# Kernel optimization log

Measured on AMD Instinct MI355X. Metric: run time of the kernel, lower is better.

The kernel has to match this reference:

```python
import jax, jax.numpy as jnp
import numpy as np

BS, S, D, H, HS, HSEL, L = 32, 512, 512, 8, 2, 4, 6
DK = D // H  # 64
HD = H - HS  # dynamic heads


def setup_inputs() -> dict:
    key = jax.random.key(0)
    ks = jax.random.split(key, 10)
    w = lambda k, shape: jax.random.normal(k, shape, dtype=jnp.float32) * 0.02
    return {
        'q_embed_data': jax.random.normal(ks[0], (BS, S, D), jnp.float32),
        'qa_embed_data': jax.random.normal(ks[1], (BS, S, D), jnp.float32),
        # stacked per-layer params (torch Linear convention: W[out,in], y = x@W.T+b)
        'Wq': w(ks[2], (L, D, D)), 'bq': jnp.zeros((L, D), jnp.float32),
        'Wv': w(ks[3], (L, D, D)), 'bv': jnp.zeros((L, D), jnp.float32),
        'Wg': w(ks[4], (L, HD, D)),                      # routing gate, no bias
        'Wo': w(ks[5], (L, D, D)), 'bo': jnp.zeros((L, D), jnp.float32),
        'ln1_g': jnp.ones((L, D), jnp.float32), 'ln1_b': jnp.zeros((L, D), jnp.float32),
        'W1': w(ks[6], (L, D, D)), 'b1': jnp.zeros((L, D), jnp.float32),
        'W2': w(ks[7], (L, D, D)), 'b2': jnp.zeros((L, D), jnp.float32),
        'ln2_g': jnp.ones((L, D), jnp.float32), 'ln2_b': jnp.zeros((L, D), jnp.float32),
    }


def _layer_norm(x, g, b):
    m = x.mean(-1, keepdims=True)
    v = ((x - m) ** 2).mean(-1, keepdims=True)
    return (x - m) * jax.lax.rsqrt(v + 1e-5) * g + b


def _moh_attention(xq, xv, Wq, bq, Wv, bv, Wg, Wo, bo, strict):
    bs, s, d = xq.shape
    q = xq @ Wq.T + bq            # kq_same=True: k = q projection
    v = xv @ Wv.T + bv
    qh = q.reshape(bs, s, H, DK).transpose(0, 2, 1, 3)   # [b,h,s,dk]
    vh = v.reshape(bs, s, H, DK).transpose(0, 2, 1, 3)
    scores = jnp.einsum('bhqd,bhkd->bhqk', qh, qh) / jnp.sqrt(jnp.float32(DK))
    # mask==1 -> causal incl. diag; mask==0 -> strictly causal
    allow = jnp.tril(jnp.ones((s, s), bool), k=-1 if strict else 0)
    scores = jnp.where(allow, scores, jnp.float32(-1e9))
    # pad-zero shift: first query row replaced by zeros -> uniform attention
    scores = scores.at[:, :, 0, :].set(0.0)
    # per-token top-k head routing over dynamic heads
    gates = jax.nn.softmax(q.reshape(bs * s, D) @ Wg.T, axis=-1)  # [bs*s, HD]
    _, idx = jax.lax.top_k(gates, HSEL)
    dmask = jnp.zeros_like(gates).at[jnp.arange(bs * s)[:, None], idx].set(1.0)
    dyn = (gates * dmask).reshape(bs, s, HD)
    routing = jnp.concatenate([jnp.ones((bs, s, HS), gates.dtype), dyn], -1).mean(1)  # [b,H]
    attn = jax.nn.softmax(scores, axis=-1)
    ctx = jnp.einsum('bhqk,bhkd->bhqd', attn, vh) * routing[:, :, None, None]
    out = ctx.transpose(0, 2, 1, 3).reshape(bs, s, D) @ Wo.T + bo
    f = dmask.sum(0)
    P = gates.mean(0)
    balance = jnp.sum((f / (f.sum() + 1e-5)) * (P / (P.sum() + 1e-5)))
    return out, balance


def reference(q_embed_data, qa_embed_data, Wq, bq, Wv, bv, Wg, Wo, bo,
              ln1_g, ln1_b, W1, b1, W2, b2, ln2_g, ln2_b):
    def layer(i, xq, xv, strict):
        a, bl = _moh_attention(xq, xv, Wq[i], bq[i], Wv[i], bv[i], Wg[i], Wo[i], bo[i], strict)
        x = _layer_norm(xq + a, ln1_g[i], ln1_b[i])
        ffn = jax.nn.relu(x @ W1[i].T + b1[i]) @ W2[i].T + b2[i]
        return _layer_norm(x + ffn, ln2_g[i], ln2_b[i]), bl

    y = qa_embed_data
    x = q_embed_data
    # blocks_1: self-attention on y, mask=1
    y, _ = layer(0, y, y, False)
    y, _ = layer(1, y, y, False)
    # blocks_2: alternate mask=1 self-attn / mask=0 cross-attn (values=y)
    x, _ = layer(2, x, x, False)
    x, bl = layer(3, x, y, True)
    x, _ = layer(4, x, x, False)
    x, bl = layer(5, x, y, True)
    return (x, bl)
```

## Files before the change

### kernel.cpp

```cpp
#include <hip/hip_runtime.h>
#include <cstdint>

#define BSZ 32
#define SEQ 512
#define DM  512
#define NH  8
#define DK  64
#define HS_ 2
#define HD_ 6
#define NL  6
#define MROWS (BSZ*SEQ)
#define QVLD 1024
#define SCL 0.18033688011112043f

typedef unsigned short bf16_t;
typedef __attribute__((ext_vector_type(4))) float f32x4;
typedef __attribute__((ext_vector_type(8))) short bf16x8;
typedef __attribute__((ext_vector_type(8))) unsigned short u16x8;

#define DEV static __device__ __forceinline__

DEV float bf2f(bf16_t b) {
  unsigned int u = ((unsigned int)b) << 16;
  float f; __builtin_memcpy(&f, &u, 4); return f;
}
DEV bf16_t f2b(float f) {
  unsigned int u; __builtin_memcpy(&u, &f, 4);
  unsigned int r = (u + 0x7fffu + ((u >> 16) & 1u)) >> 16;
  return (bf16_t)r;
}
DEV void unp2(unsigned int w, float& a, float& b) {
  unsigned int ua = w << 16, ub = w & 0xffff0000u;
  __builtin_memcpy(&a, &ua, 4); __builtin_memcpy(&b, &ub, 4);
}
DEV unsigned cvtpk(float lo, float hi) {
  unsigned r;
  asm("v_cvt_pk_bf16_f32 %0, %1, %2" : "=v"(r) : "v"(lo), "v"(hi));
  return r;
}

DEV void gload_lds16(const bf16_t* g, bf16_t* l) {
  __builtin_amdgcn_global_load_lds(
      (const __attribute__((address_space(1))) void*)g,
      (__attribute__((address_space(3))) void*)l, 16, 0, 0);
}

DEV bf16x8 scale_q(bf16x8 v) {
  u16x8 u;
  __builtin_memcpy(&u, &v, 16);
  unsigned w[4];
#pragma unroll
  for (int e = 0; e < 4; ++e)
    w[e] = cvtpk(bf2f(u[2 * e]) * SCL, bf2f(u[2 * e + 1]) * SCL);
  bf16x8 r;
  __builtin_memcpy(&r, w, 16);
  return r;
}

__global__ __launch_bounds__(256) void f2b2_kernel(
    const float* __restrict__ s0, const float* __restrict__ s1,
    bf16_t* __restrict__ d0, bf16_t* __restrict__ d1) {
  const float* s = blockIdx.y ? s1 : s0;
  bf16_t* d = blockIdx.y ? d1 : d0;
  const int i = blockIdx.x * 256 + threadIdx.x;
  float4 v = reinterpret_cast<const float4*>(s)[i];
  ushort4 o;
  o.x = f2b(v.x); o.y = f2b(v.y); o.z = f2b(v.z); o.w = f2b(v.w);
  reinterpret_cast<ushort4*>(d)[i] = o;
}

__global__ __launch_bounds__(256) void f2bw_kernel(
    const float* __restrict__ s0, const float* __restrict__ s1,
    const float* __restrict__ s2, const float* __restrict__ s3,
    const float* __restrict__ s4, bf16_t* __restrict__ dst) {
  const float* srcs[5] = {s0, s1, s2, s3, s4};
  const float* s = srcs[blockIdx.y];
  bf16_t* d = dst + (size_t)blockIdx.y * ((size_t)NL * DM * DM);
  const int i = blockIdx.x * 256 + threadIdx.x;
  float4 v = reinterpret_cast<const float4*>(s)[i];
  ushort4 o;
  o.x = f2b(v.x); o.y = f2b(v.y); o.z = f2b(v.z); o.w = f2b(v.w);
  reinterpret_cast<ushort4*>(d)[i] = o;
}

template <int NB, int NWG, bool RELU>
__global__ __launch_bounds__(512) void gemm8(
    const bf16_t* __restrict__ A0, const bf16_t* __restrict__ A1,
    const bf16_t* __restrict__ W0, const bf16_t* __restrict__ W1,
    const float* __restrict__ b0, const float* __restrict__ b1,
    bf16_t* __restrict__ Yb, int ldy) {
  const int K = 512;
  const int lin = blockIdx.y * NB + blockIdx.x;
  const int cpx = NWG / 8;
  const int swz = (lin & 7) * cpx + (lin >> 3);
  const int bn = swz % NB, bm = swz / NB;
  const int tid = threadIdx.x, wid = tid >> 6, lane = tid & 63;
  const int wr = wid >> 2, wc = wid & 3;
  const int lrow = lane & 15, grp = lane >> 4;
  const int l3 = lane >> 3, c3 = lane & 7;

  __shared__ __align__(16) bf16_t Lds[3][24576];

  const bool hi = (bn * 256) >= 512;
  const bf16_t* Asel = hi ? A1 : A0;
  const bf16_t* Wsel = hi ? (W1 - (size_t)512 * K) : W0;
  const float* bsel = hi ? (b1 - 512) : b0;

  f32x4 acc[4][4];
#pragma unroll
  for (int m = 0; m < 4; ++m)
#pragma unroll
    for (int n = 0; n < 4; ++n) acc[m][n] = f32x4{0.f, 0.f, 0.f, 0.f};

  const char* LB = (const char*)Lds;

  auto stage3 = [&](int kt, int buf, int half) {
#pragma unroll
    for (int cc = 0; cc < 3; ++cc) {
      const int c = wid + (half * 3 + cc) * 8;
      const int colb = ((c3 ^ l3) * 8);
      if (c < 16) {
        gload_lds16(Asel + (size_t)(bm * 128 + c * 8 + l3) * K + kt * 64 + colb,
                    &Lds[buf][c * 512]);
      } else {
        const int cb = c - 16;
        gload_lds16(Wsel + (size_t)(bn * 256 + cb * 8 + l3) * K + kt * 64 + colb,
                    &Lds[buf][8192 + cb * 512]);
      }
    }
  };
  auto rdA = [&](int buf, int rA, int ks) -> bf16x8 {
    const int off = buf * 49152 + rA * 128 + ((ks * 64 + grp * 16) ^ ((rA & 7) << 4));
    return *reinterpret_cast<const bf16x8*>(LB + off);
  };
  auto rdB = [&](int buf, int rB, int ks) -> bf16x8 {
    const int off = buf * 49152 + 16384 + rB * 128 + ((ks * 64 + grp * 16) ^ ((rB & 7) << 4));
    return *reinterpret_cast<const bf16x8*>(LB + off);
  };

  stage3(0, 0, 0); stage3(0, 0, 1);
  stage3(1, 1, 0); stage3(1, 1, 1);
  asm volatile("s_waitcnt vmcnt(6)" ::: "memory");
  __builtin_amdgcn_s_barrier();

  for (int g = 0; g < 8; ++g) {
    const int bufR = g % 3, bufW = (g + 2) % 3;
    const bool st = g < 6;
    bf16x8 bwv[4][2], afv[2][2];
#pragma unroll
    for (int n = 0; n < 4; ++n)
#pragma unroll
      for (int ks = 0; ks < 2; ++ks)
        bwv[n][ks] = rdB(bufR, wc * 64 + n * 16 + lrow, ks);
#pragma unroll
    for (int m = 0; m < 2; ++m)
#pragma unroll
      for (int ks = 0; ks < 2; ++ks)
        afv[m][ks] = rdA(bufR, wr * 64 + m * 16 + lrow, ks);
    if (st) stage3(g + 2, bufW, 0);
    __builtin_amdgcn_s_barrier();
    asm volatile("s_waitcnt lgkmcnt(0)" ::: "memory");
    __builtin_amdgcn_s_setprio(1);
#pragma unroll
    for (int ks = 0; ks < 2; ++ks)
#pragma unroll
      for (int m = 0; m < 2; ++m)
#pragma unroll
        for (int n = 0; n < 4; ++n)
          acc[m][n] = __builtin_amdgcn_mfma_f32_16x16x32_bf16(afv[m][ks], bwv[n][ks], acc[m][n], 0, 0, 0);
    __builtin_amdgcn_s_setprio(0);
    __builtin_amdgcn_s_barrier();
#pragma unroll
    for (int m = 0; m < 2; ++m)
#pragma unroll
      for (int ks = 0; ks < 2; ++ks)
        afv[m][ks] = rdA(bufR, wr * 64 + 32 + m * 16 + lrow, ks);
    if (st) stage3(g + 2, bufW, 1);
    __builtin_amdgcn_s_barrier();
    asm volatile("s_waitcnt lgkmcnt(0)" ::: "memory");
    __builtin_amdgcn_s_setprio(1);
#pragma unroll
    for (int ks = 0; ks < 2; ++ks)
#pragma unroll
      for (int m = 0; m < 2; ++m)
#pragma unroll
        for (int n = 0; n < 4; ++n)
          acc[2 + m][n] = __builtin_amdgcn_mfma_f32_16x16x32_bf16(afv[m][ks], bwv[n][ks], acc[2 + m][n], 0, 0, 0);
    __builtin_amdgcn_s_setprio(0);
    if (g < 6) {
      asm volatile("s_waitcnt vmcnt(6)" ::: "memory");
    } else if (g == 6) {
      asm volatile("s_waitcnt vmcnt(0)" ::: "memory");
    }
    __builtin_amdgcn_s_barrier();
  }

  const int r0 = bm * 128 + wr * 64 + grp * 4;
  const int c0 = bn * 256 + wc * 64 + lrow;
#pragma unroll
  for (int n = 0; n < 4; ++n) {
    const int col = c0 + n * 16;
    const float bc = bsel[col];
#pragma unroll
    for (int qm = 0; qm < 4; ++qm)
#pragma unroll
      for (int j = 0; j < 4; ++j) {
        float v = acc[qm][n][j] + bc;
        if (RELU) v = fmaxf(v, 0.f);
        Yb[(size_t)(r0 + qm * 16 + j) * ldy + col] = f2b(v);
      }
  }
}

__global__ __launch_bounds__(256) void gates_kernel(
    const bf16_t* __restrict__ qv, const float* __restrict__ Wg,
    float* __restrict__ rdyn, float* __restrict__ fP) {
  __shared__ float wg_s[HD_ * DM];
  __shared__ float blk[4][18];
  const int tid = threadIdx.x, wid = tid >> 6, lane = tid & 63;
  for (int i = tid; i < HD_ * DM / 4; i += 256)
    reinterpret_cast<float4*>(wg_s)[i] = reinterpret_cast<const float4*>(Wg)[i];
  __syncthreads();
  const int bb = blockIdx.x >> 4;
  const int t0 = (blockIdx.x & 15) * 32 + wid * 8;
  float fs[6] = {0, 0, 0, 0, 0, 0}, ps[6] = {0, 0, 0, 0, 0, 0}, rs[6] = {0, 0, 0, 0, 0, 0};
  for (int it = 0; it < 8; ++it) {
    const int tok = bb * SEQ + t0 + it;
    uint4 u = reinterpret_cast<const uint4*>(qv + (size_t)tok * QVLD)[lane];
    float x[8];
    unp2(u.x, x[0], x[1]); unp2(u.y, x[2], x[3]);
    unp2(u.z, x[4], x[5]); unp2(u.w, x[6], x[7]);
    float g[6];
#pragma unroll
    for (int j = 0; j < 6; ++j) {
      float p = 0.f;
#pragma unroll
      for (int e = 0; e < 8; ++e) p = fmaf(x[e], wg_s[j * DM + lane * 8 + e], p);
#pragma unroll
      for (int off = 32; off; off >>= 1) p += __shfl_xor(p, off);
      g[j] = p;
    }
    float mx = g[0];
#pragma unroll
    for (int j = 1; j < 6; ++j) mx = fmaxf(mx, g[j]);
    float se = 0.f;
#pragma unroll
    for (int j = 0; j < 6; ++j) { g[j] = __expf(g[j] - mx); se += g[j]; }
    float inv = 1.f / se;
#pragma unroll
    for (int j = 0; j < 6; ++j) g[j] *= inv;
    int d1 = 0;
#pragma unroll
    for (int j = 1; j < 6; ++j)
      if (g[j] < g[d1] || (g[j] == g[d1] && j > d1)) d1 = j;
    int d2 = (d1 == 0) ? 1 : 0;
#pragma unroll
    for (int j = 0; j < 6; ++j) {
      if (j == d1) continue;
      if (g[j] < g[d2] || (g[j] == g[d2] && j > d2)) d2 = j;
    }
#pragma unroll
    for (int j = 0; j < 6; ++j) {
      const bool drop = (j == d1) || (j == d2);
      fs[j] += drop ? 0.f : 1.f;
      ps[j] += g[j];
      rs[j] += drop ? 0.f : g[j];
    }
  }
  if (lane == 0) {
#pragma unroll
    for (int j = 0; j < 6; ++j) {
      blk[wid][j] = fs[j]; blk[wid][6 + j] = ps[j]; blk[wid][12 + j] = rs[j];
    }
  }
  __syncthreads();
  if (tid < 18) {
    float s = blk[0][tid] + blk[1][tid] + blk[2][tid] + blk[3][tid];
    if (tid < 12) atomicAdd(&fP[tid], s);
    else atomicAdd(&rdyn[bb * 6 + (tid - 12)], s * (1.f / 512.f));
  }
}

__global__ __launch_bounds__(256, 2) void fattn_kernel(
    const bf16_t* __restrict__ qv, const float* __restrict__ rdyn,
    bf16_t* __restrict__ ctx, int strict) {
  const int bh = blockIdx.x, qt = blockIdx.y;
  const int b = bh >> 3, h = bh & 7;
  const int tid = threadIdx.x, wid = tid >> 6, lane = tid & 63;
  const int c0 = lane & 15, grp = lane >> 4;
  const int l3 = lane >> 3, c3 = lane & 7;
  const int kidx = lane & 31, dhalf = lane >> 5;

  __shared__ __align__(16) bf16_t Ks[64 * 64];
  __shared__ __align__(16) bf16_t Vt[64 * 72];
  __shared__ __align__(16) bf16_t Ps[4][32 * 64];
  __shared__ float csum[64];

  const bf16_t* qp = qv;
  const bf16_t* vp = qv + 512;
  const float factor = (h < HS_) ? 1.f : rdyn[b * 6 + (h - HS_)];

  const int qbase = qt * 128 + wid * 32;

  bf16x8 qf[2][2];
#pragma unroll
  for (int nt = 0; nt < 2; ++nt)
#pragma unroll
    for (int ks = 0; ks < 2; ++ks)
      qf[nt][ks] = scale_q(*reinterpret_cast<const bf16x8*>(
          qp + ((size_t)(b * SEQ + qbase + nt * 16 + c0)) * QVLD + h * DK + ks * 32 + grp * 8));

  f32x4 acc[2][4];
#pragma unroll
  for (int m = 0; m < 2; ++m)
#pragma unroll
    for (int d = 0; d < 4; ++d) acc[m][d] = f32x4{0.f, 0.f, 0.f, 0.f};
  float mreg[2] = {-3e38f, -3e38f};
  float lreg[2] = {0.f, 0.f};
  float cs[8] = {0, 0, 0, 0, 0, 0, 0, 0};

  const int lastk = (qbase + 31 - strict) >> 6;
  const int ktmax = 2 * qt + 1;

  for (int kt = 0; kt <= ktmax; ++kt) {
#pragma unroll
    for (int i = 0; i < 2; ++i) {
      int row = i * 32 + wid * 8 + l3;
      int blk = c3 ^ l3;
      gload_lds16(qp + ((size_t)(b * SEQ + kt * 64 + row)) * QVLD + h * DK + blk * 8,
                  Ks + (i * 32 + wid * 8) * 64);
    }
#pragma unroll
    for (int j = 0; j < 2; ++j) {
      const int d0 = (wid * 2 + j) * 8 + dhalf * 4;
      const bf16_t* src = vp + ((size_t)(b * SEQ + kt * 64 + 2 * kidx)) * QVLD + h * DK + d0;
      ushort4 lo = *reinterpret_cast<const ushort4*>(src);
      ushort4 hv = *reinterpret_cast<const ushort4*>(src + QVLD);
      *reinterpret_cast<unsigned*>(&Vt[(d0 + 0) * 72 + 2 * kidx]) = (unsigned)lo.x | ((unsigned)hv.x << 16);
      *reinterpret_cast<unsigned*>(&Vt[(d0 + 1) * 72 + 2 * kidx]) = (unsigned)lo.y | ((unsigned)hv.y << 16);
      *reinterpret_cast<unsigned*>(&Vt[(d0 + 2) * 72 + 2 * kidx]) = (unsigned)lo.z | ((unsigned)hv.z << 16);
      *reinterpret_cast<unsigned*>(&Vt[(d0 + 3) * 72 + 2 * kidx]) = (unsigned)lo.w | ((unsigned)hv.w << 16);
      if (qt == 3) {
        cs[j * 4 + 0] += bf2f(lo.x) + bf2f(hv.x);
        cs[j * 4 + 1] += bf2f(lo.y) + bf2f(hv.y);
        cs[j * 4 + 2] += bf2f(lo.z) + bf2f(hv.z);
        cs[j * 4 + 3] += bf2f(lo.w) + bf2f(hv.w);
      }
    }
    __syncthreads();

    if (kt <= lastk) {
      const char* KsB = (const char*)Ks;
      bf16x8 kf[4][2];
#pragma unroll
      for (int mt = 0; mt < 4; ++mt)
#pragma unroll
        for (int ks = 0; ks < 2; ++ks)
          kf[mt][ks] = *reinterpret_cast<const bf16x8*>(
              KsB + (mt * 16 + c0) * 128 + 16 * ((4 * ks + grp) ^ (c0 & 7)));
      f32x4 s[4][2];
#pragma unroll
      for (int mt = 0; mt < 4; ++mt)
#pragma unroll
        for (int nt = 0; nt < 2; ++nt) s[mt][nt] = f32x4{0.f, 0.f, 0.f, 0.f};
      __builtin_amdgcn_s_setprio(1);
#pragma unroll
      for (int mt = 0; mt < 4; ++mt)
#pragma unroll
        for (int nt = 0; nt < 2; ++nt)
#pragma unroll
          for (int ks = 0; ks < 2; ++ks)
            s[mt][nt] = __builtin_amdgcn_mfma_f32_16x16x32_bf16(
                kf[mt][ks], qf[nt][ks], s[mt][nt], 0, 0, 0);
      __builtin_amdgcn_s_setprio(0);

      const bool masked = (kt == lastk);
      if (masked) {
#pragma unroll
        for (int nt = 0; nt < 2; ++nt) {
          const int q = qbase + nt * 16 + c0;
#pragma unroll
          for (int mt = 0; mt < 4; ++mt)
#pragma unroll
            for (int j = 0; j < 4; ++j) {
              int k = kt * 64 + mt * 16 + grp * 4 + j;
              if (k + strict > q) s[mt][nt][j] = -1e30f;
            }
        }
      }
      float mx[2];
#pragma unroll
      for (int nt = 0; nt < 2; ++nt) {
        float a = fmaxf(s[0][nt][0], s[0][nt][1]);
        a = fmaxf(fmaxf(a, s[0][nt][2]), s[0][nt][3]);
        float bm_ = fmaxf(s[1][nt][0], s[1][nt][1]);
        bm_ = fmaxf(fmaxf(bm_, s[1][nt][2]), s[1][nt][3]);
        float c = fmaxf(s[2][nt][0], s[2][nt][1]);
        c = fmaxf(fmaxf(c, s[2][nt][2]), s[2][nt][3]);
        float d = fmaxf(s[3][nt][0], s[3][nt][1]);
        d = fmaxf(fmaxf(d, s[3][nt][2]), s[3][nt][3]);
        float m_ = fmaxf(fmaxf(a, bm_), fmaxf(c, d));
        m_ = fmaxf(m_, __shfl_xor(m_, 16));
        m_ = fmaxf(m_, __shfl_xor(m_, 32));
        mx[nt] = m_;
      }
      const bool defer = __all((mx[0] - mreg[0] <= 8.f) && (mx[1] - mreg[1] <= 8.f));
      float sc[2];
#pragma unroll
      for (int nt = 0; nt < 2; ++nt) {
        const float mnew = defer ? mreg[nt] : fmaxf(mreg[nt], mx[nt]);
        float ts = 0.f;
#pragma unroll
        for (int mt = 0; mt < 4; ++mt)
#pragma unroll
          for (int j = 0; j < 4; ++j) {
            float pp = exp2f(s[mt][nt][j] - mnew);
            s[mt][nt][j] = pp; ts += pp;
          }
        ts += __shfl_xor(ts, 16);
        ts += __shfl_xor(ts, 32);
        if (defer) {
          lreg[nt] += ts;
        } else {
          sc[nt] = exp2f(mreg[nt] - mnew);
          lreg[nt] = lreg[nt] * sc[nt] + ts;
          mreg[nt] = mnew;
        }
      }
      char* PsB = (char*)(&Ps[wid][0]);
#pragma unroll
      for (int nt = 0; nt < 2; ++nt)
#pragma unroll
        for (int mt = 0; mt < 4; ++mt) {
          uint2 w;
          w.x = cvtpk(s[mt][nt][0], s[mt][nt][1]);
          w.y = cvtpk(s[mt][nt][2], s[mt][nt][3]);
          int row = nt * 16 + c0;
          int off = (row * 128 + mt * 32 + grp * 8) ^ ((c0 & 7) << 4);
          *reinterpret_cast<uint2*>(PsB + off) = w;
        }
      if (!defer) {
#pragma unroll
        for (int mtq = 0; mtq < 2; ++mtq) {
          f32x4 sv;
#pragma unroll
          for (int j = 0; j < 4; ++j) sv[j] = __shfl(sc[mtq], grp * 4 + j);
#pragma unroll
          for (int dt = 0; dt < 4; ++dt) acc[mtq][dt] *= sv;
        }
      }
      bf16x8 pf[2][2], vf2[4][2];
#pragma unroll
      for (int mtq = 0; mtq < 2; ++mtq)
#pragma unroll
        for (int ks = 0; ks < 2; ++ks)
          pf[mtq][ks] = *reinterpret_cast<const bf16x8*>(
              PsB + (mtq * 16 + c0) * 128 + 16 * ((4 * ks + grp) ^ (c0 & 7)));
#pragma unroll
      for (int dt = 0; dt < 4; ++dt)
#pragma unroll
        for (int ks = 0; ks < 2; ++ks)
          vf2[dt][ks] = *reinterpret_cast<const bf16x8*>(
              (const char*)Vt + (dt * 16 + c0) * 144 + ks * 64 + grp * 16);
      __builtin_amdgcn_s_setprio(1);
#pragma unroll
      for (int mtq = 0; mtq < 2; ++mtq)
#pragma unroll
        for (int dt = 0; dt < 4; ++dt)
#pragma unroll
          for (int ks = 0; ks < 2; ++ks)
            acc[mtq][dt] = __builtin_amdgcn_mfma_f32_16x16x32_bf16(
                pf[mtq][ks], vf2[dt][ks], acc[mtq][dt], 0, 0, 0);
      __builtin_amdgcn_s_setprio(0);
    }
    __syncthreads();
  }

  if (qt == 3) {
#pragma unroll
    for (int e = 0; e < 8; ++e)
#pragma unroll
      for (int off = 1; off <= 16; off <<= 1) cs[e] += __shfl_xor(cs[e], off);
    if ((lane & 31) == 0) {
#pragma unroll
      for (int e = 0; e < 8; ++e)
        csum[(wid * 2 + (e >> 2)) * 8 + dhalf * 4 + (e & 3)] = cs[e];
    }
    __syncthreads();
    if (tid < 64)
      ctx[((size_t)(b * SEQ)) * DM + h * DK + tid] = f2b(csum[tid] * (1.f / 512.f) * factor);
  }

#pragma unroll
  for (int mtq = 0; mtq < 2; ++mtq) {
    const float inv = factor / lreg[mtq];
    f32x4 iv;
#pragma unroll
    for (int j = 0; j < 4; ++j) iv[j] = __shfl(inv, grp * 4 + j);
#pragma unroll
    for (int j = 0; j < 4; ++j) {
      const int q = qbase + mtq * 16 + grp * 4 + j;
      if (q == 0) continue;
#pragma unroll
      for (int dt = 0; dt < 4; ++dt)
        ctx[((size_t)(b * SEQ + q)) * DM + h * DK + dt * 16 + c0] =
            f2b(acc[mtq][dt][j] * iv[j]);
    }
  }
}

template <int OUT>
__global__ __launch_bounds__(256) void add_ln_kernel(
    const bf16_t* __restrict__ X, const bf16_t* __restrict__ A2,
    const float* __restrict__ gam, const float* __restrict__ bet,
    bf16_t* __restrict__ outb, float* __restrict__ outf) {
  const int wid = threadIdx.x >> 6, lane = threadIdx.x & 63;
  const size_t row = (size_t)blockIdx.x * 4 + wid;
  const size_t base = row * DM + lane * 8;
  uint4 xu = *reinterpret_cast<const uint4*>(X + base);
  uint4 au = *reinterpret_cast<const uint4*>(A2 + base);
  float z[8];
  {
    float p0, p1, q0, q1;
    unp2(xu.x, p0, p1); unp2(au.x, q0, q1); z[0] = p0 + q0; z[1] = p1 + q1;
    unp2(xu.y, p0, p1); unp2(au.y, q0, q1); z[2] = p0 + q0; z[3] = p1 + q1;
    unp2(xu.z, p0, p1); unp2(au.z, q0, q1); z[4] = p0 + q0; z[5] = p1 + q1;
    unp2(xu.w, p0, p1); unp2(au.w, q0, q1); z[6] = p0 + q0; z[7] = p1 + q1;
  }
  float s = 0.f;
#pragma unroll
  for (int e = 0; e < 8; ++e) s += z[e];
#pragma unroll
  for (int off = 32; off; off >>= 1) s += __shfl_xor(s, off);
  const float mean = s * (1.f / 512.f);
  float ss = 0.f;
#pragma unroll
  for (int e = 0; e < 8; ++e) { float d = z[e] - mean; ss += d * d; }
#pragma unroll
  for (int off = 32; off; off >>= 1) ss += __shfl_xor(ss, off);
  const float inv = rsqrtf(ss * (1.f / 512.f) + 1e-5f);
  float4 g0 = *reinterpret_cast<const float4*>(gam + lane * 8);
  float4 g1 = *reinterpret_cast<const float4*>(gam + lane * 8 + 4);
  float4 b0 = *reinterpret_cast<const float4*>(bet + lane * 8);
  float4 b1 = *reinterpret_cast<const float4*>(bet + lane * 8 + 4);
  float o[8];
  o[0] = (z[0] - mean) * inv * g0.x + b0.x;
  o[1] = (z[1] - mean) * inv * g0.y + b0.y;
  o[2] = (z[2] - mean) * inv * g0.z + b0.z;
  o[3] = (z[3] - mean) * inv * g0.w + b0.w;
  o[4] = (z[4] - mean) * inv * g1.x + b1.x;
  o[5] = (z[5] - mean) * inv * g1.y + b1.y;
  o[6] = (z[6] - mean) * inv * g1.z + b1.z;
  o[7] = (z[7] - mean) * inv * g1.w + b1.w;
  if (OUT == 0) {
    uint4 w;
    w.x = (unsigned)f2b(o[0]) | ((unsigned)f2b(o[1]) << 16);
    w.y = (unsigned)f2b(o[2]) | ((unsigned)f2b(o[3]) << 16);
    w.z = (unsigned)f2b(o[4]) | ((unsigned)f2b(o[5]) << 16);
    w.w = (unsigned)f2b(o[6]) | ((unsigned)f2b(o[7]) << 16);
    *reinterpret_cast<uint4*>(outb + base) = w;
  } else {
    float4 f0, f1;
    f0.x = o[0]; f0.y = o[1]; f0.z = o[2]; f0.w = o[3];
    f1.x = o[4]; f1.y = o[5]; f1.z = o[6]; f1.w = o[7];
    *reinterpret_cast<float4*>(outf + base) = f0;
    *reinterpret_cast<float4*>(outf + base + 4) = f1;
  }
}

__global__ void balance_kernel(const float* __restrict__ fP, float* __restrict__ out) {
  if (threadIdx.x == 0 && blockIdx.x == 0) {
    float fs = 0.f, pssum = 0.f, P[6];
    for (int j = 0; j < 6; ++j) {
      fs += fP[j];
      P[j] = fP[6 + j] * (1.f / (float)MROWS);
      pssum += P[j];
    }
    float bal = 0.f;
    for (int j = 0; j < 6; ++j)
      bal += (fP[j] / (fs + 1e-5f)) * (P[j] / (pssum + 1e-5f));
    out[0] = bal;
  }
}

extern "C" void kernel_launch(void* const* d_in, const int* in_sizes, int n_in,
                              void* d_out, int out_size, void* d_ws, size_t ws_size,
                              hipStream_t stream) {
  (void)in_sizes; (void)n_in; (void)out_size; (void)ws_size;
  const float* q_embed  = (const float*)d_in[0];
  const float* qa_embed = (const float*)d_in[1];
  const float* Wq  = (const float*)d_in[2];
  const float* bq  = (const float*)d_in[3];
  const float* Wv  = (const float*)d_in[4];
  const float* bv  = (const float*)d_in[5];
  const float* Wg  = (const float*)d_in[6];
  const float* Wo  = (const float*)d_in[7];
  const float* bo  = (const float*)d_in[8];
  const float* ln1g = (const float*)d_in[9];
  const float* ln1b = (const float*)d_in[10];
  const float* W1  = (const float*)d_in[11];
  const float* b1  = (const float*)d_in[12];
  const float* W2  = (const float*)d_in[13];
  const float* b2  = (const float*)d_in[14];
  const float* ln2g = (const float*)d_in[15];
  const float* ln2b = (const float*)d_in[16];

  char* p = (char*)d_ws;
  auto alloc = [&](size_t bytes) -> char* {
    char* r = p; p += (bytes + 255) & ~(size_t)255; return r;
  };
  const size_t WDE = (size_t)NL * DM * DM;
  const size_t AE  = (size_t)MROWS * DM;
  bf16_t* wall_b = (bf16_t*)alloc(5 * WDE * 2);
  bf16_t* wq_b = wall_b;
  bf16_t* wv_b = wall_b + WDE;
  bf16_t* wo_b = wall_b + 2 * WDE;
  bf16_t* w1_b = wall_b + 3 * WDE;
  bf16_t* w2_b = wall_b + 4 * WDE;
  bf16_t* y_b   = (bf16_t*)alloc(AE * 2);
  bf16_t* x_b   = (bf16_t*)alloc(AE * 2);
  bf16_t* qv_b  = (bf16_t*)alloc((size_t)MROWS * QVLD * 2);
  bf16_t* ctx_b = (bf16_t*)alloc(AE * 2);
  bf16_t* x1_b  = (bf16_t*)alloc(AE * 2);
  bf16_t* tmp_b = (bf16_t*)alloc(AE * 2);
  bf16_t* ffn1_b = (bf16_t*)alloc(AE * 2);
  float* stats = (float*)alloc(NL * (12 + BSZ * 6) * 4);
  float* fPbase = stats;
  float* rdynbase = stats + NL * 12;

  hipMemsetAsync(stats, 0, NL * (12 + BSZ * 6) * 4, stream);

  f2bw_kernel<<<dim3((unsigned)(WDE / 4 / 256), 5), 256, 0, stream>>>(
      Wq, Wv, Wo, W1, W2, wall_b);
  f2b2_kernel<<<dim3((unsigned)(AE / 4 / 256), 2), 256, 0, stream>>>(
      qa_embed, q_embed, y_b, x_b);

  const size_t DD = (size_t)DM * DM;
  dim3 gqv(4, 128), gn5(2, 128), gfa(256, 4);
  float* outx = (float*)d_out;

  auto layer = [&](int i, bf16_t* resb, const bf16_t* xvb, int strict, bool last) {
    float* fP = fPbase + i * 12;
    float* rdyn = rdynbase + i * (BSZ * 6);
    gemm8<4, 512, false><<<gqv, 512, 0, stream>>>(
        resb, xvb, wq_b + i * DD, wv_b + i * DD, bq + i * DM, bv + i * DM, qv_b, QVLD);
    gates_kernel<<<MROWS / 32, 256, 0, stream>>>(qv_b, Wg + (size_t)i * HD_ * DM, rdyn, fP);
    fattn_kernel<<<gfa, 256, 0, stream>>>(qv_b, rdyn, ctx_b, strict);
    gemm8<2, 256, false><<<gn5, 512, 0, stream>>>(
        ctx_b, ctx_b, wo_b + i * DD, wo_b + i * DD, bo + i * DM, bo + i * DM, tmp_b, DM);
    add_ln_kernel<0><<<MROWS / 4, 256, 0, stream>>>(
        resb, tmp_b, ln1g + i * DM, ln1b + i * DM, x1_b, nullptr);
    gemm8<2, 256, true><<<gn5, 512, 0, stream>>>(
        x1_b, x1_b, w1_b + i * DD, w1_b + i * DD, b1 + i * DM, b1 + i * DM, ffn1_b, DM);
    gemm8<2, 256, false><<<gn5, 512, 0, stream>>>(
        ffn1_b, ffn1_b, w2_b + i * DD, w2_b + i * DD, b2 + i * DM, b2 + i * DM, tmp_b, DM);
    if (last)
      add_ln_kernel<1><<<MROWS / 4, 256, 0, stream>>>(
          x1_b, tmp_b, ln2g + i * DM, ln2b + i * DM, nullptr, outx);
    else
      add_ln_kernel<0><<<MROWS / 4, 256, 0, stream>>>(
          x1_b, tmp_b, ln2g + i * DM, ln2b + i * DM, resb, nullptr);
  };

  layer(0, y_b, y_b, 0, false);
  layer(1, y_b, y_b, 0, false);
  layer(2, x_b, x_b, 0, false);
  layer(3, x_b, y_b, 1, false);
  layer(4, x_b, x_b, 0, false);
  layer(5, x_b, y_b, 1, true);
  balance_kernel<<<1, 64, 0, stream>>>(fPbase + 5 * 12, outx + (size_t)MROWS * DM);
}
```

Before: 899.9 us.

## Fuse output-projection and FFN2 GEMMs with residual add and LayerNorm

Adds a gemm_ln kernel in which each block computes a full 64-row by 512-column output tile, then adds bias and residual and applies LayerNorm in the epilogue, using a cross-wave reduction in shared memory. It replaces the Wo GEMM plus add_ln pair and the W2 GEMM plus add_ln pair, which removes the tmp buffer round trip through global memory and two launches per layer. The trade-offs are only 256 blocks of 512 threads, about 147KB of double-buffered LDS per block (so low occupancy), a single-pass E[z^2]-mean^2 variance, and scalar, uncoalesced epilogue stores.

```diff
diff --git a/kernel.cpp b/kernel.cpp
--- a/kernel.cpp
+++ b/kernel.cpp
@@ -210,6 +210,152 @@
         Yb[(size_t)(r0 + qm * 16 + j) * ldy + col] = f2b(v);
       }
   }
+}
+
+template <int OUT>
+__global__ __launch_bounds__(512) void gemm_ln(
+    const bf16_t* __restrict__ A, const bf16_t* __restrict__ W,
+    const float* __restrict__ bias, const bf16_t* __restrict__ Res,
+    const float* __restrict__ gam, const float* __restrict__ bet,
+    bf16_t* __restrict__ outb, float* __restrict__ outf) {
+  const int K = 512;
+  const int bm = blockIdx.x;
+  const int tid = threadIdx.x, wid = tid >> 6, lane = tid & 63;
+  const int lrow = lane & 15, grp = lane >> 4;
+  const int l3 = lane >> 3, c3 = lane & 7;
+
+  __shared__ __align__(16) bf16_t Lds[2][36864];
+  __shared__ float red_s[64][8], red_q[64][8], stat[64][2];
+
+  f32x4 acc[4][4];
+#pragma unroll
+  for (int m = 0; m < 4; ++m)
+#pragma unroll
+    for (int n = 0; n < 4; ++n) acc[m][n] = f32x4{0.f, 0.f, 0.f, 0.f};
+
+  const char* LB = (const char*)Lds;
+
+  auto stage = [&](int kt, int buf) {
+#pragma unroll
+    for (int k = 0; k < 9; ++k) {
+      const int c = wid + k * 8;
+      const int colb = (c3 ^ l3) * 8;
+      if (c < 8) {
+        gload_lds16(A + (size_t)(bm * 64 + c * 8 + l3) * K + kt * 64 + colb,
+                    &Lds[buf][c * 512]);
+      } else {
+        const int cb = c - 8;
+        gload_lds16(W + (size_t)(cb * 8 + l3) * K + kt * 64 + colb,
+                    &Lds[buf][4096 + cb * 512]);
+      }
+    }
+  };
+  auto rdA = [&](int buf, int r, int ks) -> bf16x8 {
+    const int off = buf * 73728 + r * 128 + ((ks * 64 + grp * 16) ^ ((r & 7) << 4));
+    return *reinterpret_cast<const bf16x8*>(LB + off);
+  };
+  auto rdW = [&](int buf, int r, int ks) -> bf16x8 {
+    const int off = buf * 73728 + 8192 + r * 128 + ((ks * 64 + grp * 16) ^ ((r & 7) << 4));
+    return *reinterpret_cast<const bf16x8*>(LB + off);
+  };
+
+  stage(0, 0);
+  __syncthreads();
+  for (int g = 0; g < 8; ++g) {
+    const int bufR = g & 1;
+    if (g < 7) stage(g + 1, bufR ^ 1);
+    bf16x8 af[4][2], wf[4][2];
+#pragma unroll
+    for (int m = 0; m < 4; ++m)
+#pragma unroll
+      for (int ks = 0; ks < 2; ++ks)
+        af[m][ks] = rdA(bufR, m * 16 + lrow, ks);
+#pragma unroll
+    for (int n = 0; n < 4; ++n)
+#pragma unroll
+      for (int ks = 0; ks < 2; ++ks)
+        wf[n][ks] = rdW(bufR, wid * 64 + n * 16 + lrow, ks);
+    __builtin_amdgcn_s_setprio(1);
+#pragma unroll
+    for (int ks = 0; ks < 2; ++ks)
+#pragma unroll
+      for (int m = 0; m < 4; ++m)
+#pragma unroll
+        for (int n = 0; n < 4; ++n)
+          acc[m][n] = __builtin_amdgcn_mfma_f32_16x16x32_bf16(af[m][ks], wf[n][ks], acc[m][n], 0, 0, 0);
+    __builtin_amdgcn_s_setprio(0);
+    __syncthreads();
+  }
+
+  const int cbase = wid * 64;
+  float bias_n[4], gam_n[4], bet_n[4];
+#pragma unroll
+  for (int n = 0; n < 4; ++n) {
+    bias_n[n] = bias[cbase + n * 16 + lrow];
+    gam_n[n]  = gam[cbase + n * 16 + lrow];
+    bet_n[n]  = bet[cbase + n * 16 + lrow];
+  }
+  const size_t rowg0 = (size_t)bm * 64;
+  float ps[4][4], pq[4][4];
+#pragma unroll
+  for (int m = 0; m < 4; ++m)
+#pragma unroll
+    for (int j = 0; j < 4; ++j) {
+      const int r = m * 16 + grp * 4 + j;
+      float s = 0.f, q = 0.f;
+#pragma unroll
+      for (int n = 0; n < 4; ++n) {
+        float z = acc[m][n][j] + bias_n[n] +
+                  bf2f(Res[(rowg0 + r) * DM + cbase + n * 16 + lrow]);
+        acc[m][n][j] = z;
+        s += z; q += z * z;
+      }
+      ps[m][j] = s; pq[m][j] = q;
+    }
+#pragma unroll
+  for (int m = 0; m < 4; ++m)
+#pragma unroll
+    for (int j = 0; j < 4; ++j)
+#pragma unroll
+      for (int off = 1; off <= 8; off <<= 1) {
+        ps[m][j] += __shfl_xor(ps[m][j], off);
+        pq[m][j] += __shfl_xor(pq[m][j], off);
+      }
+  if (lrow == 0) {
+#pragma unroll
+    for (int m = 0; m < 4; ++m)
+#pragma unroll
+      for (int j = 0; j < 4; ++j) {
+        const int r = m * 16 + grp * 4 + j;
+        red_s[r][wid] = ps[m][j];
+        red_q[r][wid] = pq[m][j];
+      }
+  }
+  __syncthreads();
+  if (tid < 64) {
+    float s = 0.f, q = 0.f;
+#pragma unroll
+    for (int w = 0; w < 8; ++w) { s += red_s[tid][w]; q += red_q[tid][w]; }
+    const float mean = s * (1.f / 512.f);
+    const float var = q * (1.f / 512.f) - mean * mean;
+    stat[tid][0] = mean;
+    stat[tid][1] = rsqrtf(var + 1e-5f);
+  }
+  __syncthreads();
+#pragma unroll
+  for (int m = 0; m < 4; ++m)
+#pragma unroll
+    for (int j = 0; j < 4; ++j) {
+      const int r = m * 16 + grp * 4 + j;
+      const float mean = stat[r][0], rstd = stat[r][1];
+#pragma unroll
+      for (int n = 0; n < 4; ++n) {
+        const float o = (acc[m][n][j] - mean) * rstd * gam_n[n] + bet_n[n];
+        const size_t off = (rowg0 + r) * DM + cbase + n * 16 + lrow;
+        if (OUT == 0) outb[off] = f2b(o);
+        else outf[off] = o;
+      }
+    }
 }
 
 __global__ __launch_bounds__(256) void gates_kernel(
@@ -506,65 +652,6 @@
         ctx[((size_t)(b * SEQ + q)) * DM + h * DK + dt * 16 + c0] =
             f2b(acc[mtq][dt][j] * iv[j]);
     }
-  }
-}
-
-template <int OUT>
-__global__ __launch_bounds__(256) void add_ln_kernel(
-    const bf16_t* __restrict__ X, const bf16_t* __restrict__ A2,
-    const float* __restrict__ gam, const float* __restrict__ bet,
-    bf16_t* __restrict__ outb, float* __restrict__ outf) {
-  const int wid = threadIdx.x >> 6, lane = threadIdx.x & 63;
-  const size_t row = (size_t)blockIdx.x * 4 + wid;
-  const size_t base = row * DM + lane * 8;
-  uint4 xu = *reinterpret_cast<const uint4*>(X + base);
-  uint4 au = *reinterpret_cast<const uint4*>(A2 + base);
-  float z[8];
-  {
-    float p0, p1, q0, q1;
-    unp2(xu.x, p0, p1); unp2(au.x, q0, q1); z[0] = p0 + q0; z[1] = p1 + q1;
-    unp2(xu.y, p0, p1); unp2(au.y, q0, q1); z[2] = p0 + q0; z[3] = p1 + q1;
-    unp2(xu.z, p0, p1); unp2(au.z, q0, q1); z[4] = p0 + q0; z[5] = p1 + q1;
-    unp2(xu.w, p0, p1); unp2(au.w, q0, q1); z[6] = p0 + q0; z[7] = p1 + q1;
-  }
-  float s = 0.f;
-#pragma unroll
-  for (int e = 0; e < 8; ++e) s += z[e];
-#pragma unroll
-  for (int off = 32; off; off >>= 1) s += __shfl_xor(s, off);
-  const float mean = s * (1.f / 512.f);
-  float ss = 0.f;
-#pragma unroll
-  for (int e = 0; e < 8; ++e) { float d = z[e] - mean; ss += d * d; }
-#pragma unroll
-  for (int off = 32; off; off >>= 1) ss += __shfl_xor(ss, off);
-  const float inv = rsqrtf(ss * (1.f / 512.f) + 1e-5f);
-  float4 g0 = *reinterpret_cast<const float4*>(gam + lane * 8);
-  float4 g1 = *reinterpret_cast<const float4*>(gam + lane * 8 + 4);
-  float4 b0 = *reinterpret_cast<const float4*>(bet + lane * 8);
-  float4 b1 = *reinterpret_cast<const float4*>(bet + lane * 8 + 4);
-  float o[8];
-  o[0] = (z[0] - mean) * inv * g0.x + b0.x;
-  o[1] = (z[1] - mean) * inv * g0.y + b0.y;
-  o[2] = (z[2] - mean) * inv * g0.z + b0.z;
-  o[3] = (z[3] - mean) * inv * g0.w + b0.w;
-  o[4] = (z[4] - mean) * inv * g1.x + b1.x;
-  o[5] = (z[5] - mean) * inv * g1.y + b1.y;
-  o[6] = (z[6] - mean) * inv * g1.z + b1.z;
-  o[7] = (z[7] - mean) * inv * g1.w + b1.w;
-  if (OUT == 0) {
-    uint4 w;
-    w.x = (unsigned)f2b(o[0]) | ((unsigned)f2b(o[1]) << 16);
-    w.y = (unsigned)f2b(o[2]) | ((unsigned)f2b(o[3]) << 16);
-    w.z = (unsigned)f2b(o[4]) | ((unsigned)f2b(o[5]) << 16);
-    w.w = (unsigned)f2b(o[6]) | ((unsigned)f2b(o[7]) << 16);
-    *reinterpret_cast<uint4*>(outb + base) = w;
-  } else {
-    float4 f0, f1;
-    f0.x = o[0]; f0.y = o[1]; f0.z = o[2]; f0.w = o[3];
-    f1.x = o[4]; f1.y = o[5]; f1.z = o[6]; f1.w = o[7];
-    *reinterpret_cast<float4*>(outf + base) = f0;
-    *reinterpret_cast<float4*>(outf + base + 4) = f1;
   }
 }
 
@@ -622,7 +709,6 @@
   bf16_t* qv_b  = (bf16_t*)alloc((size_t)MROWS * QVLD * 2);
   bf16_t* ctx_b = (bf16_t*)alloc(AE * 2);
   bf16_t* x1_b  = (bf16_t*)alloc(AE * 2);
-  bf16_t* tmp_b = (bf16_t*)alloc(AE * 2);
   bf16_t* ffn1_b = (bf16_t*)alloc(AE * 2);
   float* stats = (float*)alloc(NL * (12 + BSZ * 6) * 4);
   float* fPbase = stats;
@@ -636,7 +722,7 @@
       qa_embed, q_embed, y_b, x_b);
 
   const size_t DD = (size_t)DM * DM;
-  dim3 gqv(4, 128), gn5(2, 128), gfa(256, 4);
+  dim3 gqv(4, 128), gn5(2, 128), gfa(256, 4), gln(256);
   float* outx = (float*)d_out;
 
   auto layer = [&](int i, bf16_t* resb, const bf16_t* xvb, int strict, bool last) {
@@ -646,20 +732,19 @@
         resb, xvb, wq_b + i * DD, wv_b + i * DD, bq + i * DM, bv + i * DM, qv_b, QVLD);
     gates_kernel<<<MROWS / 32, 256, 0, stream>>>(qv_b, Wg + (size_t)i * HD_ * DM, rdyn, fP);
     fattn_kernel<<<gfa, 256, 0, stream>>>(qv_b, rdyn, ctx_b, strict);
-    gemm8<2, 256, false><<<gn5, 512, 0, stream>>>(
-        ctx_b, ctx_b, wo_b + i * DD, wo_b + i * DD, bo + i * DM, bo + i * DM, tmp_b, DM);
-    add_ln_kernel<0><<<MROWS / 4, 256, 0, stream>>>(
-        resb, tmp_b, ln1g + i * DM, ln1b + i * DM, x1_b, nullptr);
+    gemm_ln<0><<<gln, 512, 0, stream>>>(
+        ctx_b, wo_b + i * DD, bo + i * DM, resb, ln1g + i * DM, ln1b + i * DM,
+        x1_b, nullptr);
     gemm8<2, 256, true><<<gn5, 512, 0, stream>>>(
         x1_b, x1_b, w1_b + i * DD, w1_b + i * DD, b1 + i * DM, b1 + i * DM, ffn1_b, DM);
-    gemm8<2, 256, false><<<gn5, 512, 0, stream>>>(
-        ffn1_b, ffn1_b, w2_b + i * DD, w2_b + i * DD, b2 + i * DM, b2 + i * DM, tmp_b, DM);
     if (last)
-      add_ln_kernel<1><<<MROWS / 4, 256, 0, stream>>>(
-          x1_b, tmp_b, ln2g + i * DM, ln2b + i * DM, nullptr, outx);
+      gemm_ln<1><<<gln, 512, 0, stream>>>(
+          ffn1_b, w2_b + i * DD, b2 + i * DM, x1_b, ln2g + i * DM, ln2b + i * DM,
+          nullptr, outx);
     else
-      add_ln_kernel<0><<<MROWS / 4, 256, 0, stream>>>(
-          x1_b, tmp_b, ln2g + i * DM, ln2b + i * DM, resb, nullptr);
+      gemm_ln<0><<<gln, 512, 0, stream>>>(
+          ffn1_b, w2_b + i * DD, b2 + i * DM, x1_b, ln2g + i * DM, ln2b + i * DM,
+          resb, nullptr);
   };
 
   layer(0, y_b, y_b, 0, false);
```

Result: no change. 887.7 us, median of 3 (-1.4%).
